# Kernel tuning notes

Hardware: AMD Instinct MI355X
Metric: run time of the kernel (lower is better)

## Reference

```python
import jax, jax.numpy as jnp
import numpy as np

B, S, D, H, L, V = 2, 512, 1024, 16, 12, 50257
HD = D // H
DFF = 4 * D


def _ln(x, g, b, eps=1e-5):
    m = jnp.mean(x, axis=-1, keepdims=True)
    v = jnp.var(x, axis=-1, keepdims=True)
    return (x - m) * jax.lax.rsqrt(v + eps) * g + b


def setup_inputs() -> dict:
    key = jax.random.key(0)
    ks = jax.random.split(key, 32)
    sc = 0.02
    n = lambda k, shape: (jax.random.normal(k, shape, dtype=jnp.float32) * sc)
    inp = {
        "input_ids": jax.random.randint(ks[0], (B, S), 0, V, dtype=jnp.int64),
        "attention_mask": jnp.ones((B, S), dtype=jnp.float32),
        "image_hidden_states": jax.random.normal(ks[1], (B, D), dtype=jnp.float32),
        # token embedding table (also used for position embeds and tied lm_head, as in source)
        "wte": n(ks[2], (V, D)),
        # feature_space_transformation_nn: Linear(1024,1024) -> ReLU -> Linear(1024,1024)
        "ft_W1": n(ks[3], (D, D)), "ft_b1": jnp.zeros((D,), jnp.float32),
        "ft_W2": n(ks[4], (D, D)), "ft_b2": jnp.zeros((D,), jnp.float32),
        # per-layer params, stacked on leading L dim
        "ln1_g": jnp.ones((L, D), jnp.float32), "ln1_b": jnp.zeros((L, D), jnp.float32),
        "Wattn": n(ks[5], (L, D, 3 * D)), "battn": jnp.zeros((L, 3 * D), jnp.float32),
        "Wuk": n(ks[6], (L, D, D)), "buk": jnp.zeros((L, D), jnp.float32),
        "Wuv": n(ks[7], (L, D, D)), "buv": jnp.zeros((L, D), jnp.float32),
        "Wproj": n(ks[8], (L, D, D)), "bproj": jnp.zeros((L, D), jnp.float32),
        "ln2_g": jnp.ones((L, D), jnp.float32), "ln2_b": jnp.zeros((L, D), jnp.float32),
        "Wfc": n(ks[9], (L, D, DFF)), "bfc": jnp.zeros((L, DFF), jnp.float32),
        "Wfc2": n(ks[10], (L, DFF, D)), "bfc2": jnp.zeros((L, D), jnp.float32),
        "lnf_g": jnp.ones((D,), jnp.float32), "lnf_b": jnp.zeros((D,), jnp.float32),
    }
    return inp


def _forward(input_ids, attention_mask, image_hidden_states, wte,
             ft_W1, ft_b1, ft_W2, ft_b2,
             ln1_g, ln1_b, Wattn, battn, Wuk, buk, Wuv, buv, Wproj, bproj,
             ln2_g, ln2_b, Wfc, bfc, Wfc2, bfc2, lnf_g, lnf_b):
    # image feature transformation: Linear -> ReLU -> Linear
    img = jax.nn.relu(image_hidden_states @ ft_W1 + ft_b1) @ ft_W2 + ft_b2  # [B,D]

    # NOTE: source uses wte (not wpe) for position embeddings — faithful reproduction
    h = wte[input_ids] + wte[jnp.arange(S)][None]  # [B,S,D]

    # extended attention mask with a prepended zero column for the image token
    mask_ext = (1.0 - attention_mask)[:, None, None, :] * -10000.0  # [B,1,1,S]
    mask_ext = jnp.concatenate([jnp.zeros((B, 1, 1, 1), mask_ext.dtype), mask_ext], axis=-1)  # [B,1,1,S+1]

    # causal mask over kv_len=S+1: query i sees keys j <= i+1 (image token always visible)
    causal = jnp.arange(S + 1)[None, :] <= (jnp.arange(S)[:, None] + 1)  # [S,S+1]

    def block(h, p):
        (l1g, l1b, Wa, ba, Wk, bk, Wv, bv, Wp, bp, l2g, l2b, Wf, bf, Wf2, bf2) = p
        x = _ln(h, l1g, l1b)
        qkv = x @ Wa + ba
        q, k, v = jnp.split(qkv, 3, axis=-1)  # each [B,S,D]
        ki = (img @ Wk + bk)[:, None, :]  # [B,1,D]
        vi = (img @ Wv + bv)[:, None, :]
        k = jnp.concatenate([ki, k], axis=1)  # [B,S+1,D]
        v = jnp.concatenate([vi, v], axis=1)
        sh = lambda t, n: t.reshape(B, n, H, HD).transpose(0, 2, 1, 3)
        qh, kh, vh = sh(q, S), sh(k, S + 1), sh(v, S + 1)
        s = jnp.einsum('bhqd,bhkd->bhqk', qh, kh) / jnp.sqrt(jnp.float32(HD))
        s = jnp.where(causal[None, None], s, jnp.float32(-10000.0))
        s = s + mask_ext
        a = jax.nn.softmax(s, axis=-1)
        o = jnp.einsum('bhqk,bhkd->bhqd', a, vh).transpose(0, 2, 1, 3).reshape(B, S, D)
        h = h + (o @ Wp + bp)
        x = _ln(h, l2g, l2b)
        h = h + (jax.nn.gelu(x @ Wf + bf, approximate=True) @ Wf2 + bf2)
        return h, None

    params = (ln1_g, ln1_b, Wattn, battn, Wuk, buk, Wuv, buv, Wproj, bproj,
              ln2_g, ln2_b, Wfc, bfc, Wfc2, bfc2)
    h, _ = jax.lax.scan(block, h, params)
    h = _ln(h, lnf_g, lnf_b)
    return h @ wte.T  # tied lm head -> [B,S,V]


def reference(input_ids, attention_mask, image_hidden_states, wte,
              ft_W1, ft_b1, ft_W2, ft_b2,
              ln1_g, ln1_b, Wattn, battn, Wuk, buk, Wuv, buv, Wproj, bproj,
              ln2_g, ln2_b, Wfc, bfc, Wfc2, bfc2, lnf_g, lnf_b):
    return _forward(input_ids, attention_mask, image_hidden_states, wte,
                    ft_W1, ft_b1, ft_W2, ft_b2,
                    ln1_g, ln1_b, Wattn, battn, Wuk, buk, Wuv, buv, Wproj, bproj,
                    ln2_g, ln2_b, Wfc, bfc, Wfc2, bfc2, lnf_g, lnf_b)
```

## Files before the change

### kernel.cpp

```cpp
#include <hip/hip_runtime.h>
#include <cstdint>


typedef __bf16 bf16x8 __attribute__((ext_vector_type(8)));
typedef __bf16 bf16x4 __attribute__((ext_vector_type(4)));
typedef float  f32x4  __attribute__((ext_vector_type(4)));

#define GLDS16(g, l) __builtin_amdgcn_global_load_lds( \
    (const __attribute__((address_space(1))) unsigned int*)(g), \
    (__attribute__((address_space(3))) unsigned int*)(l), 16, 0, 0)

#define SCHED_FENCE() __builtin_amdgcn_sched_barrier(0)

__device__ __forceinline__ float gelu_f(float x) {
    float u = 1.5957691216057308f * (x + 0.044715f * x * x * x);
    float e = __expf(u);
    float t = 1.0f - 2.0f / (e + 1.0f);
    return 0.5f * x * (1.0f + t);
}

__device__ __forceinline__ int fragoff(int row, int kh, int hi) {
    return row * 64 + ((kh * 32 + hi * 8) ^ ((row & 7) << 3));
}
__device__ __forceinline__ int fragoff32(int row, int hi) {
    return row * 32 + ((hi * 8) ^ ((row & 3) << 3));
}

__device__ __forceinline__ void tcvt_body(
    int id, const float* __restrict__ Wa, const float* __restrict__ Wp,
    const float* __restrict__ Wf, const float* __restrict__ Wf2,
    __bf16* __restrict__ oa, __bf16* __restrict__ op,
    __bf16* __restrict__ of, __bf16* __restrict__ of2, float* tile)
{
    const float* src; __bf16* dst; int K, N, kb, nb;
    if (id < 768)       { src = Wa;  dst = oa;  K = 1024; N = 3072; kb = id & 15; nb = id >> 4; }
    else if (id < 1024) { id -= 768;  src = Wp;  dst = op;  K = 1024; N = 1024; kb = id & 15; nb = id >> 4; }
    else if (id < 2048) { id -= 1024; src = Wf;  dst = of;  K = 1024; N = 4096; kb = id & 15; nb = id >> 4; }
    else                { id -= 2048; src = Wf2; dst = of2; K = 4096; N = 1024; kb = id & 63; nb = id >> 6; }
    const int k0 = kb * 64, n0 = nb * 64;
    const int t = threadIdx.x;
    #pragma unroll
    for (int i = 0; i < 4; i++) {
        int r = i * 16 + (t >> 4), c = (t & 15) * 4;
        float4 v = *reinterpret_cast<const float4*>(src + (long)(k0 + r) * N + n0 + c);
        tile[r * 65 + c] = v.x; tile[r * 65 + c + 1] = v.y;
        tile[r * 65 + c + 2] = v.z; tile[r * 65 + c + 3] = v.w;
    }
    __syncthreads();
    const int nrow = t >> 2, kc = (t & 3) * 16;
    bf16x8 o0, o1;
    #pragma unroll
    for (int i = 0; i < 8; i++) {
        o0[i] = (__bf16)tile[(kc + i) * 65 + nrow];
        o1[i] = (__bf16)tile[(kc + 8 + i) * 65 + nrow];
    }
    *reinterpret_cast<bf16x8*>(dst + (long)(n0 + nrow) * K + k0 + kc)     = o0;
    *reinterpret_cast<bf16x8*>(dst + (long)(n0 + nrow) * K + k0 + kc + 8) = o1;
}

__device__ __forceinline__ void wcvt_body(
    int id, const float* __restrict__ wte, __bf16* __restrict__ out, long nvalid)
{
    long base = (long)id * 8192 + threadIdx.x * 8;
    #pragma unroll
    for (int i = 0; i < 4; i++) {
        long e = base + (long)i * 2048;
        bf16x8 o;
        if (e < nvalid) {
            float4 a = *reinterpret_cast<const float4*>(wte + e);
            float4 b = *reinterpret_cast<const float4*>(wte + e + 4);
            o[0] = (__bf16)a.x; o[1] = (__bf16)a.y; o[2] = (__bf16)a.z; o[3] = (__bf16)a.w;
            o[4] = (__bf16)b.x; o[5] = (__bf16)b.y; o[6] = (__bf16)b.z; o[7] = (__bf16)b.w;
        } else {
            #pragma unroll
            for (int q = 0; q < 8; q++) o[q] = (__bf16)0.f;
        }
        *reinterpret_cast<bf16x8*>(out + e) = o;
    }
}

__global__ __launch_bounds__(256) void tcvt_std(
    const float* __restrict__ Wa, const float* __restrict__ Wp,
    const float* __restrict__ Wf, const float* __restrict__ Wf2,
    __bf16* __restrict__ oa, __bf16* __restrict__ op,
    __bf16* __restrict__ of, __bf16* __restrict__ of2)
{
    __shared__ float tile[64 * 65];
    tcvt_body(blockIdx.x, Wa, Wp, Wf, Wf2, oa, op, of, of2, tile);
}

__global__ __launch_bounds__(256) void wcvt_std(
    const float* __restrict__ wte, __bf16* __restrict__ out, long nvalid)
{
    wcvt_body(blockIdx.x, wte, out, nvalid);
}

__global__ __launch_bounds__(256) void gemv_part(
    const float* __restrict__ x, int xld,
    const float* __restrict__ W, long wzs,
    float* __restrict__ part, int K, int N)
{
    int jb = blockIdx.x, kz = blockIdx.y, z = blockIdx.z;
    int t = threadIdx.x;
    int j = (jb << 6) + (t & 63);
    int g = t >> 6;
    int klen = K / (gridDim.y * 4);
    int kbase = (kz * 4 + g) * klen;
    const float* Wp = W + (long)z * wzs + (long)kbase * N + j;
    const float* x0 = x + kbase;
    const float* x1 = x + xld + kbase;
    float a0 = 0.f, a1 = 0.f;
    for (int k = 0; k < klen; k++) {
        float wv = Wp[(long)k * N];
        a0 += x0[k] * wv;
        a1 += x1[k] * wv;
    }
    __shared__ float r0[4][64], r1[4][64];
    r0[g][t & 63] = a0; r1[g][t & 63] = a1;
    __syncthreads();
    if (t < 64) {
        a0 = r0[0][t] + r0[1][t] + r0[2][t] + r0[3][t];
        a1 = r1[0][t] + r1[1][t] + r1[2][t] + r1[3][t];
        long base = (long)(z * gridDim.y + kz) * 2 * N + (jb << 6) + t;
        part[base]     = a0;
        part[base + N] = a1;
    }
}

__global__ __launch_bounds__(256) void gemv_reduce(
    const float* __restrict__ part, const float* __restrict__ bias, long bzs,
    float* __restrict__ out, int N, int nz, int act)
{
    int idx = blockIdx.x * 256 + threadIdx.x;
    if (idx >= nz * 2 * N) return;
    int j  = idx % N;
    int bz = idx / N;
    int z  = bz >> 1;
    float s = bias[(long)z * bzs + j];
    const float* p = part + ((long)z * 8 * 2 + (bz & 1)) * N + j;
    #pragma unroll
    for (int kz = 0; kz < 8; kz++) s += p[(long)kz * 2 * N];
    if (act) s = fmaxf(s, 0.f);
    out[idx] = s;
}

__global__ __launch_bounds__(256) void gemv_kv_part(
    const float* __restrict__ img,
    const float* __restrict__ Wuk, const float* __restrict__ Wuv,
    float* __restrict__ part)
{
    int jb = blockIdx.x, kz = blockIdx.y, z = blockIdx.z;
    int t = threadIdx.x;
    int j = (jb << 6) + (t & 63);
    int g = t >> 6;
    int kbase = (kz * 4 + g) * 64;
    const float* W = (z < 12) ? (Wuk + (long)z * 1048576) : (Wuv + (long)(z - 12) * 1048576);
    const float* Wp = W + (long)kbase * 1024 + j;
    const float* x0 = img + kbase;
    const float* x1 = img + 1024 + kbase;
    float a0 = 0.f, a1 = 0.f;
    for (int k = 0; k < 64; k++) {
        float wv = Wp[(long)k * 1024];
        a0 += x0[k] * wv;
        a1 += x1[k] * wv;
    }
    __shared__ float r0[4][64], r1[4][64];
    r0[g][t & 63] = a0; r1[g][t & 63] = a1;
    __syncthreads();
    if (t < 64) {
        a0 = r0[0][t] + r0[1][t] + r0[2][t] + r0[3][t];
        a1 = r1[0][t] + r1[1][t] + r1[2][t] + r1[3][t];
        long base = (long)(z * 4 + kz) * 2 * 1024 + (jb << 6) + t;
        part[base]        = a0;
        part[base + 1024] = a1;
    }
}

__global__ __launch_bounds__(256) void gemv_kv_reduce(
    const float* __restrict__ part,
    const float* __restrict__ buk, const float* __restrict__ buv,
    float* __restrict__ imgk, float* __restrict__ imgv)
{
    int idx = blockIdx.x * 256 + threadIdx.x;
    int z = idx >> 11;
    int bsel = (idx >> 10) & 1;
    int j = idx & 1023;
    float s = (z < 12) ? buk[z * 1024 + j] : buv[(z - 12) * 1024 + j];
    const float* p = part + ((long)z * 4 * 2 + bsel) * 1024 + j;
    #pragma unroll
    for (int kz = 0; kz < 4; kz++) s += p[(long)kz * 2 * 1024];
    if (z < 12) imgk[z * 2048 + bsel * 1024 + j] = s;
    else        imgv[(z - 12) * 2048 + bsel * 1024 + j] = s;
}

__global__ __launch_bounds__(256) void embed_ln(
    const int* __restrict__ ids, const float* __restrict__ wte,
    float* __restrict__ h, __bf16* __restrict__ xb,
    const float* __restrict__ g, const float* __restrict__ b)
{
    int row = blockIdx.x;
    int s = row & 511;
    int t = threadIdx.x;
    long id = ids[row];
    float4 v1 = reinterpret_cast<const float4*>(wte + id * 1024)[t];
    float4 v2 = reinterpret_cast<const float4*>(wte + (long)s * 1024)[t];
    float4 v; v.x = v1.x + v2.x; v.y = v1.y + v2.y; v.z = v1.z + v2.z; v.w = v1.w + v2.w;
    reinterpret_cast<float4*>(h + (long)row * 1024)[t] = v;

    float s1 = v.x + v.y + v.z + v.w;
    float s2 = v.x * v.x + v.y * v.y + v.z * v.z + v.w * v.w;
    #pragma unroll
    for (int o = 32; o >= 1; o >>= 1) { s1 += __shfl_xor(s1, o); s2 += __shfl_xor(s2, o); }
    __shared__ float r1[4], r2[4];
    int w = t >> 6;
    if ((t & 63) == 0) { r1[w] = s1; r2[w] = s2; }
    __syncthreads();
    s1 = r1[0] + r1[1] + r1[2] + r1[3];
    s2 = r2[0] + r2[1] + r2[2] + r2[3];
    float mean = s1 * (1.0f / 1024.0f);
    float var  = s2 * (1.0f / 1024.0f) - mean * mean;
    float rstd = rsqrtf(var + 1e-5f);
    float4 gg = reinterpret_cast<const float4*>(g)[t];
    float4 bb = reinterpret_cast<const float4*>(b)[t];
    bf16x4 o;
    o[0] = (__bf16)((v.x - mean) * rstd * gg.x + bb.x);
    o[1] = (__bf16)((v.y - mean) * rstd * gg.y + bb.y);
    o[2] = (__bf16)((v.z - mean) * rstd * gg.z + bb.z);
    o[3] = (__bf16)((v.w - mean) * rstd * gg.w + bb.w);
    *reinterpret_cast<bf16x4*>(xb + (long)row * 1024 + t * 4) = o;
}

__global__ __launch_bounds__(256) void ln_k(
    const float* __restrict__ in, __bf16* __restrict__ out,
    const float* __restrict__ g, const float* __restrict__ b)
{
    int row = blockIdx.x, t = threadIdx.x;
    float4 v = reinterpret_cast<const float4*>(in + (long)row * 1024)[t];
    float s1 = v.x + v.y + v.z + v.w;
    float s2 = v.x * v.x + v.y * v.y + v.z * v.z + v.w * v.w;
    #pragma unroll
    for (int o = 32; o >= 1; o >>= 1) { s1 += __shfl_xor(s1, o); s2 += __shfl_xor(s2, o); }
    __shared__ float r1[4], r2[4];
    int w = t >> 6;
    if ((t & 63) == 0) { r1[w] = s1; r2[w] = s2; }
    __syncthreads();
    s1 = r1[0] + r1[1] + r1[2] + r1[3];
    s2 = r2[0] + r2[1] + r2[2] + r2[3];
    float mean = s1 * (1.0f / 1024.0f);
    float var  = s2 * (1.0f / 1024.0f) - mean * mean;
    float rstd = rsqrtf(var + 1e-5f);
    float4 gg = reinterpret_cast<const float4*>(g)[t];
    float4 bb = reinterpret_cast<const float4*>(b)[t];
    bf16x4 o;
    o[0] = (__bf16)((v.x - mean) * rstd * gg.x + bb.x);
    o[1] = (__bf16)((v.y - mean) * rstd * gg.y + bb.y);
    o[2] = (__bf16)((v.z - mean) * rstd * gg.z + bb.z);
    o[3] = (__bf16)((v.w - mean) * rstd * gg.w + bb.w);
    *reinterpret_cast<bf16x4*>(out + (long)row * 1024 + t * 4) = o;
}

template<int NP>
__global__ __launch_bounds__(256) void lnadd_k(
    float* __restrict__ h, const float* __restrict__ part,
    const float* __restrict__ bias,
    const float* __restrict__ g, const float* __restrict__ b,
    __bf16* __restrict__ out)
{
    int row = blockIdx.x, t = threadIdx.x;
    long off = (long)row * 1024 + t * 4;
    float4 v = *reinterpret_cast<const float4*>(h + off);
    #pragma unroll
    for (int sp = 0; sp < NP; sp++) {
        float4 pv = *reinterpret_cast<const float4*>(part + sp * 1048576L + off);
        v.x += pv.x; v.y += pv.y; v.z += pv.z; v.w += pv.w;
    }
    float4 bi = reinterpret_cast<const float4*>(bias)[t];
    v.x += bi.x; v.y += bi.y; v.z += bi.z; v.w += bi.w;
    *reinterpret_cast<float4*>(h + off) = v;

    float s1 = v.x + v.y + v.z + v.w;
    float s2 = v.x * v.x + v.y * v.y + v.z * v.z + v.w * v.w;
    #pragma unroll
    for (int o = 32; o >= 1; o >>= 1) { s1 += __shfl_xor(s1, o); s2 += __shfl_xor(s2, o); }
    __shared__ float r1[4], r2[4];
    int w = t >> 6;
    if ((t & 63) == 0) { r1[w] = s1; r2[w] = s2; }
    __syncthreads();
    s1 = r1[0] + r1[1] + r1[2] + r1[3];
    s2 = r2[0] + r2[1] + r2[2] + r2[3];
    float mean = s1 * (1.0f / 1024.0f);
    float var  = s2 * (1.0f / 1024.0f) - mean * mean;
    float rstd = rsqrtf(var + 1e-5f);
    float4 gg = reinterpret_cast<const float4*>(g)[t];
    float4 bb = reinterpret_cast<const float4*>(b)[t];
    bf16x4 o;
    o[0] = (__bf16)((v.x - mean) * rstd * gg.x + bb.x);
    o[1] = (__bf16)((v.y - mean) * rstd * gg.y + bb.y);
    o[2] = (__bf16)((v.z - mean) * rstd * gg.z + bb.z);
    o[3] = (__bf16)((v.w - mean) * rstd * gg.w + bb.w);
    *reinterpret_cast<bf16x4*>(out + off) = o;
}

__global__ __launch_bounds__(512, 4) void gemm_lm2(
    const __bf16* __restrict__ A, const __bf16* __restrict__ Bt,
    float* __restrict__ C, int N, int K, int GM, int GN)
{
    const int total = GM * GN;
    const int q = total >> 3, r = total & 7;
    const int x = blockIdx.x & 7, jj = blockIdx.x >> 3;
    const int w0 = (x < r) ? x * (q + 1) + jj : r * (q + 1) + (x - r) * q + jj;
    const int m0 = (w0 % GM) * 128;
    const int n0 = (w0 / GM) * 256;

    __shared__ __bf16 As[2][128 * 32];
    __shared__ __bf16 Bs[2][256 * 32];
    const int t = threadIdx.x;
    const int wid = t >> 6, lane = t & 63;
    const int lo = lane & 15, hi = lane >> 4;
    const int wr = wid >> 2, wc = wid & 3;

    f32x4 acc[4][4] = {};

    const int srow = t >> 2;
    const int skx  = (((t & 3) ^ (srow & 3)) << 3);
    const int sldst = t * 8;
    #define STLM(bf, kk) do { \
        GLDS16(A + (long)(m0 + srow) * K + (kk) + skx, &As[bf][sldst]); \
        GLDS16(Bt + (long)(n0 + srow)       * K + (kk) + skx, &Bs[bf][sldst]); \
        GLDS16(Bt + (long)(n0 + 128 + srow) * K + (kk) + skx, &Bs[bf][4096 + sldst]); \
    } while (0)

    const int T = K >> 5;
    STLM(0, 0);
    int cur = 0;
    for (int it = 0; it < T; it++) {
        if (it + 1 < T) {
            STLM(cur ^ 1, (it + 1) * 32);
            asm volatile("s_waitcnt vmcnt(3)" ::: "memory");
        } else {
            asm volatile("s_waitcnt vmcnt(0)" ::: "memory");
        }
        SCHED_FENCE();
        __builtin_amdgcn_s_barrier();
        SCHED_FENCE();

        bf16x8 afr[4], bfr[4];
        #pragma unroll
        for (int mi = 0; mi < 4; mi++)
            afr[mi] = *reinterpret_cast<const bf16x8*>(&As[cur][fragoff32(wr * 64 + mi * 16 + lo, hi)]);
        #pragma unroll
        for (int ni = 0; ni < 4; ni++)
            bfr[ni] = *reinterpret_cast<const bf16x8*>(&Bs[cur][fragoff32(wc * 64 + ni * 16 + lo, hi)]);
        __builtin_amdgcn_s_setprio(1);
        #pragma unroll
        for (int mi = 0; mi < 4; mi++)
            #pragma unroll
            for (int ni = 0; ni < 4; ni++)
                acc[mi][ni] = __builtin_amdgcn_mfma_f32_16x16x32_bf16(afr[mi], bfr[ni], acc[mi][ni], 0, 0, 0);
        __builtin_amdgcn_s_setprio(0);

        SCHED_FENCE();
        __builtin_amdgcn_s_barrier();
        SCHED_FENCE();
        cur ^= 1;
    }
    #undef STLM

    #pragma unroll
    for (int mi = 0; mi < 4; mi++)
        #pragma unroll
        for (int ni = 0; ni < 4; ni++) {
            int col = n0 + wc * 64 + ni * 16 + lo;
            if (col >= N) continue;
            #pragma unroll
            for (int rr = 0; rr < 4; rr++) {
                int row = m0 + wr * 64 + mi * 16 + hi * 4 + rr;
                C[(long)row * N + col] = acc[mi][ni][rr];
            }
        }
}

template<int BN, int OUTBF16, int ACT, int PARTIAL>
__global__ __launch_bounds__(256) void gemm64(
    const __bf16* __restrict__ A, const __bf16* __restrict__ Bt,
    const float* __restrict__ bias, void* __restrict__ C,
    int N, int K, int GM, int GN, int NS)
{
    constexpr int NB = BN / 32;
    const int total = GM * GN * NS;
    const int q = total >> 3, r = total & 7;
    const int x = blockIdx.x & 7, jj = blockIdx.x >> 3;
    const int w0 = (x < r) ? x * (q + 1) + jj : r * (q + 1) + (x - r) * q + jj;
    const int sp = w0 / (GM * GN);
    const int rem = w0 - sp * (GM * GN);
    const int m0 = (rem % GM) * 64;
    const int n0 = (rem / GM) * BN;

    __shared__ __bf16 As[2][64 * 64];
    __shared__ __bf16 Bs[2][BN * 64];
    const int t = threadIdx.x;
    const int wv = t >> 6, lane = t & 63;
    const int lo = lane & 15, hi = lane >> 4;
    const int wr = wv >> 1, wc = wv & 1;

    f32x4 acc[2][NB] = {};

    const int srow = t >> 3;
    const int skx  = (((t & 7) ^ (srow & 7)) << 3);
    const int sldst = t * 8;
    #define ST64(bf, kk) do { \
        _Pragma("unroll") \
        for (int i = 0; i < 2; i++) \
            GLDS16(A + (long)(m0 + i * 32 + srow) * K + (kk) + skx, &As[bf][i * 2048 + sldst]); \
        _Pragma("unroll") \
        for (int i = 0; i < NB; i++) \
            GLDS16(Bt + (long)(n0 + i * 32 + srow) * K + (kk) + skx, &Bs[bf][i * 2048 + sldst]); \
    } while (0)

    const int Ksp = K / NS;
    const int kbeg = sp * Ksp;
    const int T = Ksp >> 6;

    ST64(0, kbeg);
    int cur = 0;
    for (int it = 0; it < T; it++) {
        if (it + 1 < T) {
            ST64(cur ^ 1, kbeg + (it + 1) * 64);
            if constexpr (NB == 4) asm volatile("s_waitcnt vmcnt(6)" ::: "memory");
            else                   asm volatile("s_waitcnt vmcnt(4)" ::: "memory");
        } else {
            asm volatile("s_waitcnt vmcnt(0)" ::: "memory");
        }
        SCHED_FENCE();
        __builtin_amdgcn_s_barrier();
        SCHED_FENCE();

        #pragma unroll
        for (int kh = 0; kh < 2; kh++) {
            bf16x8 afr[2], bfr[NB];
            #pragma unroll
            for (int mi = 0; mi < 2; mi++)
                afr[mi] = *reinterpret_cast<const bf16x8*>(&As[cur][fragoff(wr * 32 + mi * 16 + lo, kh, hi)]);
            #pragma unroll
            for (int ni = 0; ni < NB; ni++)
                bfr[ni] = *reinterpret_cast<const bf16x8*>(&Bs[cur][fragoff(wc * (BN / 2) + ni * 16 + lo, kh, hi)]);
            __builtin_amdgcn_s_setprio(1);
            #pragma unroll
            for (int mi = 0; mi < 2; mi++)
                #pragma unroll
                for (int ni = 0; ni < NB; ni++)
                    acc[mi][ni] = __builtin_amdgcn_mfma_f32_16x16x32_bf16(afr[mi], bfr[ni], acc[mi][ni], 0, 0, 0);
            __builtin_amdgcn_s_setprio(0);
        }

        SCHED_FENCE();
        __builtin_amdgcn_s_barrier();
        SCHED_FENCE();
        cur ^= 1;
    }
    #undef ST64

    const long coff = PARTIAL ? (long)sp * GM * 64 * N : 0;
    #pragma unroll
    for (int mi = 0; mi < 2; mi++)
        #pragma unroll
        for (int ni = 0; ni < NB; ni++) {
            int col = n0 + wc * (BN / 2) + ni * 16 + lo;
            float bv = (!PARTIAL && bias) ? bias[col] : 0.f;
            #pragma unroll
            for (int rr = 0; rr < 4; rr++) {
                int row = m0 + wr * 32 + mi * 16 + hi * 4 + rr;
                float v = acc[mi][ni][rr] + bv;
                if (ACT) v = gelu_f(v);
                if (OUTBF16) ((__bf16*)C)[(long)row * N + col] = (__bf16)v;
                else         ((float*)C)[coff + (long)row * N + col] = v;
            }
        }
}

template<int OUTBF16, int ACT, int RES>
__global__ __launch_bounds__(256) void gemm_bb(
    const __bf16* __restrict__ A, const __bf16* __restrict__ Bt,
    const float* __restrict__ bias, const float* __restrict__ res,
    void* __restrict__ C, int N, int K)
{
    __shared__ __bf16 As[64 * 32];
    __shared__ __bf16 Bs[64 * 32];
    const int t = threadIdx.x;
    const int m0 = blockIdx.x * 64;
    const int n0 = blockIdx.y * 64;
    const int w = t >> 6, lane = t & 63;
    const int lo = lane & 15, hi = lane >> 4;
    const int wr = w >> 1, wc = w & 1;

    f32x4 acc[2][2] = {};

    for (int k0 = 0; k0 < K; k0 += 32) {
        __syncthreads();
        GLDS16(A  + (long)(m0 + (t >> 2)) * K + k0 + ((t & 3) << 3), &As[t * 8]);
        GLDS16(Bt + (long)(n0 + (t >> 2)) * K + k0 + ((t & 3) << 3), &Bs[t * 8]);
        __syncthreads();
        bf16x8 afr[2], bfr[2];
        #pragma unroll
        for (int mi = 0; mi < 2; mi++)
            afr[mi] = *reinterpret_cast<const bf16x8*>(&As[(wr * 32 + mi * 16 + lo) * 32 + hi * 8]);
        #pragma unroll
        for (int ni = 0; ni < 2; ni++)
            bfr[ni] = *reinterpret_cast<const bf16x8*>(&Bs[(wc * 32 + ni * 16 + lo) * 32 + hi * 8]);
        #pragma unroll
        for (int mi = 0; mi < 2; mi++)
            #pragma unroll
            for (int ni = 0; ni < 2; ni++)
                acc[mi][ni] = __builtin_amdgcn_mfma_f32_16x16x32_bf16(afr[mi], bfr[ni], acc[mi][ni], 0, 0, 0);
    }

    #pragma unroll
    for (int mi = 0; mi < 2; mi++)
        #pragma unroll
        for (int ni = 0; ni < 2; ni++) {
            int col = n0 + wc * 32 + ni * 16 + lo;
            float bv = bias ? bias[col] : 0.f;
            #pragma unroll
            for (int rr = 0; rr < 4; rr++) {
                int row = m0 + wr * 32 + mi * 16 + hi * 4 + rr;
                float v = acc[mi][ni][rr] + bv;
                if (ACT) v = gelu_f(v);
                if (RES) v += res[(long)row * N + col];
                if (OUTBF16) ((__bf16*)C)[(long)row * N + col] = (__bf16)v;
                else         ((float*)C)[(long)row * N + col] = v;
            }
        }
}

__global__ __launch_bounds__(256) void gemm_lm(
    const __bf16* __restrict__ A, const float* __restrict__ Wt,
    float* __restrict__ C, int N, int K)
{
    __shared__ __bf16 As[128 * 32];
    __shared__ __bf16 Bs[128 * 32];
    const int t = threadIdx.x;
    const int m0 = blockIdx.x * 128;
    const int n0 = blockIdx.y * 128;
    const int w = t >> 6, lane = t & 63;
    const int lo = lane & 15, hi = lane >> 4;
    const int wr = w >> 1, wc = w & 1;

    f32x4 acc[4][4] = {};

    for (int k0 = 0; k0 < K; k0 += 32) {
        __syncthreads();
        #pragma unroll
        for (int i = 0; i < 2; i++) {
            int c = i * 256 + t;
            GLDS16(A + (long)(m0 + (c >> 2)) * K + k0 + ((c & 3) << 3), &As[c * 8]);
        }
        #pragma unroll
        for (int i = 0; i < 2; i++) {
            int c = i * 256 + t;
            int nr = n0 + (c >> 2);
            bf16x8 bv;
            if (nr < N) {
                const float* wp = Wt + (long)nr * K + k0 + ((c & 3) << 3);
                float4 b0 = *reinterpret_cast<const float4*>(wp);
                float4 b1 = *reinterpret_cast<const float4*>(wp + 4);
                bv[0] = (__bf16)b0.x; bv[1] = (__bf16)b0.y; bv[2] = (__bf16)b0.z; bv[3] = (__bf16)b0.w;
                bv[4] = (__bf16)b1.x; bv[5] = (__bf16)b1.y; bv[6] = (__bf16)b1.z; bv[7] = (__bf16)b1.w;
            } else {
                #pragma unroll
                for (int qq = 0; qq < 8; qq++) bv[qq] = (__bf16)0.f;
            }
            *reinterpret_cast<bf16x8*>(&Bs[c * 8]) = bv;
        }
        __syncthreads();
        bf16x8 afr[4], bfr[4];
        #pragma unroll
        for (int mi = 0; mi < 4; mi++)
            afr[mi] = *reinterpret_cast<const bf16x8*>(&As[(wr * 64 + mi * 16 + lo) * 32 + hi * 8]);
        #pragma unroll
        for (int ni = 0; ni < 4; ni++)
            bfr[ni] = *reinterpret_cast<const bf16x8*>(&Bs[(wc * 64 + ni * 16 + lo) * 32 + hi * 8]);
        #pragma unroll
        for (int mi = 0; mi < 4; mi++)
            #pragma unroll
            for (int ni = 0; ni < 4; ni++)
                acc[mi][ni] = __builtin_amdgcn_mfma_f32_16x16x32_bf16(afr[mi], bfr[ni], acc[mi][ni], 0, 0, 0);
    }

    #pragma unroll
    for (int mi = 0; mi < 4; mi++)
        #pragma unroll
        for (int ni = 0; ni < 4; ni++) {
            int col = n0 + wc * 64 + ni * 16 + lo;
            if (col < N) {
                #pragma unroll
                for (int rr = 0; rr < 4; rr++) {
                    int row = m0 + wr * 64 + mi * 16 + hi * 4 + rr;
                    C[(long)row * N + col] = acc[mi][ni][rr];
                }
            }
        }
}

__global__ __launch_bounds__(256) void attn_aux(
    const __bf16* __restrict__ qkv,
    const float* __restrict__ imgk, const float* __restrict__ imgv,
    const float* __restrict__ amask, __bf16* __restrict__ out,
    int aux_mode,
    const float* __restrict__ Wa, const float* __restrict__ Wp,
    const float* __restrict__ Wf, const float* __restrict__ Wf2,
    __bf16* __restrict__ oa, __bf16* __restrict__ op,
    __bf16* __restrict__ of, __bf16* __restrict__ of2,
    const float* __restrict__ wte, __bf16* __restrict__ wteb, long nvalid)
{
    __shared__ __align__(16) char smem[28416];
    const int bid = blockIdx.x;
    if (bid >= 256) {
        if (aux_mode == 1)
            tcvt_body(bid - 256, Wa, Wp, Wf, Wf2, oa, op, of, of2, (float*)smem);
        else
            wcvt_body(bid - 256, wte, wteb, nvalid);
        return;
    }

    __bf16 (*Ks)[72] = (__bf16(*)[72])(smem);
    __bf16 (*Vt)[72] = (__bf16(*)[72])(smem + 9216);
    __bf16 (*Ps)[16][72] = (__bf16(*)[16][72])(smem + 18432);
    float* kimg_s = (float*)(smem + 27648);
    float* amv_s  = (float*)(smem + 27904);

    const int qb = bid & 7;
    const int h  = (bid >> 3) & 15;
    const int b  = bid >> 7;
    const int t = threadIdx.x, w = t >> 6, lane = t & 63;
    const int lo = lane & 15, hi = lane >> 4;

    const int kr8 = t >> 2, kd8 = (t & 3) * 16;
    const int vr8 = t & 63, vd8 = (t >> 6) * 16;

    const __bf16* qrow = qkv + (long)(b * 512 + qb * 64 + w * 16 + lo) * 3072 + h * 64;
    bf16x8 qf0 = *reinterpret_cast<const bf16x8*>(qrow + hi * 8);
    bf16x8 qf1 = *reinterpret_cast<const bf16x8*>(qrow + 32 + hi * 8);

    if (t < 64) kimg_s[t] = imgk[b * 1024 + h * 64 + t];
    __syncthreads();

    float simg = 0.f;
    #pragma unroll
    for (int i = 0; i < 8; i++)
        simg += (float)qf0[i] * kimg_s[hi * 8 + i] + (float)qf1[i] * kimg_s[32 + hi * 8 + i];
    simg += __shfl_xor(simg, 16);
    simg += __shfl_xor(simg, 32);
    simg *= 0.125f;

    float pimg[4], l_part[4];
    f32x4 o_acc[4];
    #pragma unroll
    for (int rr = 0; rr < 4; rr++) {
        pimg[rr] = __expf(__shfl(simg, hi * 4 + rr));
        l_part[rr] = 0.f;
    }
    #pragma unroll
    for (int df = 0; df < 4; df++) {
        float vi = imgv[b * 1024 + h * 64 + df * 16 + lo];
        #pragma unroll
        for (int rr = 0; rr < 4; rr++) o_acc[df][rr] = pimg[rr] * vi;
    }

    bf16x8 ck0, ck1, cv0, cv1;
    {
        const __bf16* ks = qkv + (long)(b * 512 + kr8) * 3072 + 1024 + h * 64 + kd8;
        ck0 = *reinterpret_cast<const bf16x8*>(ks);
        ck1 = *reinterpret_cast<const bf16x8*>(ks + 8);
        const __bf16* vs = qkv + (long)(b * 512 + vr8) * 3072 + 2048 + h * 64 + vd8;
        cv0 = *reinterpret_cast<const bf16x8*>(vs);
        cv1 = *reinterpret_cast<const bf16x8*>(vs + 8);
    }

    for (int kb = 0; kb <= qb; kb++) {
        bf16x8 nk0, nk1, nv0, nv1;
        const bool more = (kb < qb);
        if (more) {
            const __bf16* ks = qkv + (long)(b * 512 + (kb + 1) * 64 + kr8) * 3072 + 1024 + h * 64 + kd8;
            nk0 = *reinterpret_cast<const bf16x8*>(ks);
            nk1 = *reinterpret_cast<const bf16x8*>(ks + 8);
            const __bf16* vs = qkv + (long)(b * 512 + (kb + 1) * 64 + vr8) * 3072 + 2048 + h * 64 + vd8;
            nv0 = *reinterpret_cast<const bf16x8*>(vs);
            nv1 = *reinterpret_cast<const bf16x8*>(vs + 8);
        }
        __syncthreads();
        *reinterpret_cast<bf16x8*>(&Ks[kr8][kd8])     = ck0;
        *reinterpret_cast<bf16x8*>(&Ks[kr8][kd8 + 8]) = ck1;
        #pragma unroll
        for (int i = 0; i < 8; i++) { Vt[vd8 + i][vr8] = cv0[i]; Vt[vd8 + 8 + i][vr8] = cv1[i]; }
        if (t < 64) amv_s[t] = (1.0f - amask[b * 512 + kb * 64 + t]) * -10000.0f;
        __syncthreads();

        f32x4 sf[4];
        #pragma unroll
        for (int js = 0; js < 4; js++) {
            bf16x8 kf0 = *reinterpret_cast<const bf16x8*>(&Ks[js * 16 + lo][hi * 8]);
            bf16x8 kf1 = *reinterpret_cast<const bf16x8*>(&Ks[js * 16 + lo][32 + hi * 8]);
            f32x4 a = {};
            a = __builtin_amdgcn_mfma_f32_16x16x32_bf16(qf0, kf0, a, 0, 0, 0);
            a = __builtin_amdgcn_mfma_f32_16x16x32_bf16(qf1, kf1, a, 0, 0, 0);
            sf[js] = a;
        }
        #pragma unroll
        for (int js = 0; js < 4; js++) {
            float amv = amv_s[js * 16 + lo];
            #pragma unroll
            for (int rr = 0; rr < 4; rr++) {
                float sv = sf[js][rr] * 0.125f + amv;
                if (kb == qb) {
                    int qrw = w * 16 + hi * 4 + rr;
                    if (js * 16 + lo > qrw) sv = -10000.0f + amv;
                }
                float p = __expf(sv);
                l_part[rr] += p;
                Ps[w][hi * 4 + rr][js * 16 + lo] = (__bf16)p;
            }
        }
        #pragma unroll
        for (int jb = 0; jb < 2; jb++) {
            bf16x8 pf = *reinterpret_cast<const bf16x8*>(&Ps[w][lo][jb * 32 + hi * 8]);
            #pragma unroll
            for (int df = 0; df < 4; df++) {
                bf16x8 vf = *reinterpret_cast<const bf16x8*>(&Vt[df * 16 + lo][jb * 32 + hi * 8]);
                o_acc[df] = __builtin_amdgcn_mfma_f32_16x16x32_bf16(pf, vf, o_acc[df], 0, 0, 0);
            }
        }
        if (more) { ck0 = nk0; ck1 = nk1; cv0 = nv0; cv1 = nv1; }
    }

    float linv[4];
    #pragma unroll
    for (int rr = 0; rr < 4; rr++) {
        float ls = l_part[rr];
        #pragma unroll
        for (int off = 1; off < 16; off <<= 1) ls += __shfl_xor(ls, off);
        linv[rr] = 1.0f / (pimg[rr] + ls);
    }
    #pragma unroll
    for (int df = 0; df < 4; df++)
        #pragma unroll
        for (int rr = 0; rr < 4; rr++) {
            long row = b * 512 + qb * 64 + w * 16 + hi * 4 + rr;
            out[row * 1024 + h * 64 + df * 16 + lo] = (__bf16)(o_acc[df][rr] * linv[rr]);
        }
}

extern "C" void kernel_launch(void* const* d_in, const int* in_sizes, int n_in,
                              void* d_out, int out_size, void* d_ws, size_t ws_size,
                              hipStream_t stream) {
    (void)in_sizes; (void)n_in; (void)out_size;
    const int*   ids   = (const int*)d_in[0];
    const float* amask = (const float*)d_in[1];
    const float* ihs   = (const float*)d_in[2];
    const float* wte   = (const float*)d_in[3];
    const float* ftW1  = (const float*)d_in[4];
    const float* ftb1  = (const float*)d_in[5];
    const float* ftW2  = (const float*)d_in[6];
    const float* ftb2  = (const float*)d_in[7];
    const float* ln1g  = (const float*)d_in[8];
    const float* ln1b  = (const float*)d_in[9];
    const float* Wattn = (const float*)d_in[10];
    const float* battn = (const float*)d_in[11];
    const float* Wuk   = (const float*)d_in[12];
    const float* buk   = (const float*)d_in[13];
    const float* Wuv   = (const float*)d_in[14];
    const float* buv   = (const float*)d_in[15];
    const float* Wproj = (const float*)d_in[16];
    const float* bproj = (const float*)d_in[17];
    const float* ln2g  = (const float*)d_in[18];
    const float* ln2b  = (const float*)d_in[19];
    const float* Wfc   = (const float*)d_in[20];
    const float* bfc   = (const float*)d_in[21];
    const float* Wfc2  = (const float*)d_in[22];
    const float* bfc2  = (const float*)d_in[23];
    const float* lnfg  = (const float*)d_in[24];
    const float* lnfb  = (const float*)d_in[25];
    float* out = (float*)d_out;

    const long VP2 = 50432;
    const long NVALID = 50257L * 1024;
    char* base = (char*)d_ws;
    float* ftmp  = (float*)(base);
    float* img   = (float*)(base + (1 << 13));
    float* imgk  = (float*)(base + (1 << 14));
    float* imgv  = (float*)(base + 114688);
    float* part  = (float*)(base + 212992);
    float* h     = (float*)(base + 1048576);
    char* p = base + 5 * 1048576;
    __bf16* xb    = (__bf16*)p; p += 2 * 1048576;
    __bf16* qkvb  = (__bf16*)p; p += 6 * 1048576;
    __bf16* attob = (__bf16*)p; p += 2 * 1048576;
    __bf16* ffb   = (__bf16*)p; p += 8 * 1048576;
    __bf16* wtA0  = (__bf16*)p; p += 6 * 1048576;
    __bf16* wtP0  = (__bf16*)p; p += 2 * 1048576;
    __bf16* wtF0  = (__bf16*)p; p += 8 * 1048576;
    __bf16* wtF20 = (__bf16*)p; p += 8 * 1048576;
    __bf16* wteb  = (__bf16*)p; p += VP2 * 1024 * 2;
    size_t need1 = (size_t)(p - base);
    float* part_g = (float*)(base + need1);
    size_t need2 = need1 + 4 * 1048576 * sizeof(float);
    char* p2 = base + need2;
    __bf16* wtA1  = (__bf16*)p2; p2 += 6 * 1048576;
    __bf16* wtP1  = (__bf16*)p2; p2 += 2 * 1048576;
    __bf16* wtF1  = (__bf16*)p2; p2 += 8 * 1048576;
    __bf16* wtF21 = (__bf16*)p2; p2 += 8 * 1048576;
    size_t need3 = (size_t)(p2 - base);
    const bool big1 = (ws_size >= need1);
    const bool big2 = (ws_size >= need2);
    const bool big3 = (ws_size >= need3);

    __bf16* wtA_s[2]  = {wtA0, wtA1};
    __bf16* wtP_s[2]  = {wtP0, wtP1};
    __bf16* wtF_s[2]  = {wtF0, wtF1};
    __bf16* wtF2_s[2] = {wtF20, wtF21};

    dim3 b256(256);

    gemv_part<<<dim3(16, 8, 1), b256, 0, stream>>>(ihs, 1024, ftW1, 0, part, 1024, 1024);
    gemv_reduce<<<dim3(8), b256, 0, stream>>>(part, ftb1, 0, ftmp, 1024, 1, 1);
    gemv_part<<<dim3(16, 8, 1), b256, 0, stream>>>(ftmp, 1024, ftW2, 0, part, 1024, 1024);
    gemv_reduce<<<dim3(8), b256, 0, stream>>>(part, ftb2, 0, img, 1024, 1, 0);
    gemv_kv_part<<<dim3(16, 4, 24), b256, 0, stream>>>(img, Wuk, Wuv, part);
    gemv_kv_reduce<<<dim3(192), b256, 0, stream>>>(part, buk, buv, imgk, imgv);

    embed_ln<<<dim3(1024), b256, 0, stream>>>(ids, wte, h, xb, ln1g, ln1b);
    tcvt_std<<<dim3(3072), b256, 0, stream>>>(
        Wattn, Wproj, Wfc, Wfc2, wtA0, wtP0, wtF0, wtF20);

    for (int l = 0; l < 12; l++) {
        const int cs = big3 ? (l & 1) : 0;
        __bf16* cA  = wtA_s[cs];
        __bf16* cP  = wtP_s[cs];
        __bf16* cF  = wtF_s[cs];
        __bf16* cF2 = wtF2_s[cs];

        if (!big3 && l > 0) {
            tcvt_std<<<dim3(3072), b256, 0, stream>>>(
                Wattn + (long)l * 1024 * 3072, Wproj + (long)l * 1024 * 1024,
                Wfc + (long)l * 1024 * 4096, Wfc2 + (long)l * 4096 * 1024,
                wtA0, wtP0, wtF0, wtF20);
        }

        gemm64<128, 1, 0, 0><<<dim3(384), b256, 0, stream>>>(
            xb, cA, battn + l * 3072, qkvb, 3072, 1024, 16, 24, 1);

        if (big3 && l < 11) {
            const int ns = (l + 1) & 1;
            attn_aux<<<dim3(256 + 3072), b256, 0, stream>>>(
                qkvb, imgk + l * 2048, imgv + l * 2048, amask, attob, 1,
                Wattn + (long)(l + 1) * 1024 * 3072, Wproj + (long)(l + 1) * 1024 * 1024,
                Wfc + (long)(l + 1) * 1024 * 4096, Wfc2 + (long)(l + 1) * 4096 * 1024,
                wtA_s[ns], wtP_s[ns], wtF_s[ns], wtF2_s[ns],
                nullptr, nullptr, 0);
        } else if (big3 && l == 11) {
            attn_aux<<<dim3(256 + 6304), b256, 0, stream>>>(
                qkvb, imgk + l * 2048, imgv + l * 2048, amask, attob, 2,
                nullptr, nullptr, nullptr, nullptr,
                nullptr, nullptr, nullptr, nullptr,
                wte, wteb, NVALID);
        } else {
            attn_aux<<<dim3(256), b256, 0, stream>>>(
                qkvb, imgk + l * 2048, imgv + l * 2048, amask, attob, 0,
                nullptr, nullptr, nullptr, nullptr,
                nullptr, nullptr, nullptr, nullptr,
                nullptr, nullptr, 0);
        }

        const float* ng = (l < 11) ? (ln1g + (l + 1) * 1024) : lnfg;
        const float* nb = (l < 11) ? (ln1b + (l + 1) * 1024) : lnfb;
        if (big2) {
            gemm64<64, 0, 0, 1><<<dim3(512), b256, 0, stream>>>(
                attob, cP, nullptr, part_g, 1024, 1024, 16, 16, 2);
            lnadd_k<2><<<dim3(1024), b256, 0, stream>>>(
                h, part_g, bproj + l * 1024, ln2g + l * 1024, ln2b + l * 1024, xb);
            gemm64<128, 1, 1, 0><<<dim3(512), b256, 0, stream>>>(
                xb, cF, bfc + l * 4096, ffb, 4096, 1024, 16, 32, 1);
            gemm64<128, 0, 0, 1><<<dim3(512), b256, 0, stream>>>(
                ffb, cF2, nullptr, part_g, 1024, 4096, 16, 8, 4);
            lnadd_k<4><<<dim3(1024), b256, 0, stream>>>(
                h, part_g, bfc2 + l * 1024, ng, nb, xb);
        } else {
            gemm_bb<0, 0, 1><<<dim3(16, 16), b256, 0, stream>>>(
                attob, cP, bproj + l * 1024, h, h, 1024, 1024);
            ln_k<<<dim3(1024), b256, 0, stream>>>(h, xb, ln2g + l * 1024, ln2b + l * 1024);
            gemm64<128, 1, 1, 0><<<dim3(512), b256, 0, stream>>>(
                xb, cF, bfc + l * 4096, ffb, 4096, 1024, 16, 32, 1);
            gemm_bb<0, 0, 1><<<dim3(16, 16), b256, 0, stream>>>(
                ffb, cF2, bfc2 + l * 1024, h, h, 1024, 4096);
            ln_k<<<dim3(1024), b256, 0, stream>>>(h, xb, ng, nb);
        }
    }

    if (big1) {
        if (!big3)
            wcvt_std<<<dim3((unsigned)(VP2 * 1024 / 8192)), b256, 0, stream>>>(wte, wteb, NVALID);
        gemm_lm2<<<dim3(8 * (int)(VP2 / 256)), dim3(512), 0, stream>>>(
            xb, wteb, out, 50257, 1024, 8, (int)(VP2 / 256));
    } else {
        gemm_lm<<<dim3(8, 393), b256, 0, stream>>>(xb, wte, out, 50257, 1024);
    }
}
```

Measured before the change: 1.477 ms.

## Triple-buffer LDS prefetch in GEMM kernels and change lm-head LDS swizzle

Both the lm-head GEMM and the generic 64-row GEMM move from double to triple buffering in shared memory, so loads for two k-steps ahead are in flight and the vmcnt wait thresholds are adjusted to match. The lm-head kernel's 32-wide LDS swizzle now XORs on (row>>1)&3 instead of row&3, aimed at reducing bank conflicts in fragment reads. The extra buffer raises LDS use per block by half, which may lower occupancy, especially for the 512-thread lm-head kernel with launch bounds of 4 blocks.

```diff
diff --git a/kernel.cpp b/kernel.cpp
--- a/kernel.cpp
+++ b/kernel.cpp
@@ -23,7 +23,7 @@
     return row * 64 + ((kh * 32 + hi * 8) ^ ((row & 7) << 3));
 }
 __device__ __forceinline__ int fragoff32(int row, int hi) {
-    return row * 32 + ((hi * 8) ^ ((row & 3) << 3));
+    return row * 32 + ((hi ^ ((row >> 1) & 3)) << 3);
 }
 
 __device__ __forceinline__ void tcvt_body(
@@ -312,8 +312,8 @@
     const int m0 = (w0 % GM) * 128;
     const int n0 = (w0 / GM) * 256;
 
-    __shared__ __bf16 As[2][128 * 32];
-    __shared__ __bf16 Bs[2][256 * 32];
+    __shared__ __bf16 As[3][128 * 32];
+    __shared__ __bf16 Bs[3][256 * 32];
     const int t = threadIdx.x;
     const int wid = t >> 6, lane = t & 63;
     const int lo = lane & 15, hi = lane >> 4;
@@ -322,7 +322,7 @@
     f32x4 acc[4][4] = {};
 
     const int srow = t >> 2;
-    const int skx  = (((t & 3) ^ (srow & 3)) << 3);
+    const int skx  = (((t & 3) ^ ((srow >> 1) & 3)) << 3);
     const int sldst = t * 8;
     #define STLM(bf, kk) do { \
         GLDS16(A + (long)(m0 + srow) * K + (kk) + skx, &As[bf][sldst]); \
@@ -332,10 +332,14 @@
 
     const int T = K >> 5;
     STLM(0, 0);
-    int cur = 0;
+    if (T > 1) STLM(1, 32);
+    int bcur = 0;
     for (int it = 0; it < T; it++) {
-        if (it + 1 < T) {
-            STLM(cur ^ 1, (it + 1) * 32);
+        if (it + 2 < T) {
+            int bst = bcur >= 1 ? bcur - 1 : bcur + 2;
+            STLM(bst, (it + 2) * 32);
+            asm volatile("s_waitcnt vmcnt(6)" ::: "memory");
+        } else if (it + 1 < T) {
             asm volatile("s_waitcnt vmcnt(3)" ::: "memory");
         } else {
             asm volatile("s_waitcnt vmcnt(0)" ::: "memory");
@@ -347,10 +351,10 @@
         bf16x8 afr[4], bfr[4];
         #pragma unroll
         for (int mi = 0; mi < 4; mi++)
-            afr[mi] = *reinterpret_cast<const bf16x8*>(&As[cur][fragoff32(wr * 64 + mi * 16 + lo, hi)]);
+            afr[mi] = *reinterpret_cast<const bf16x8*>(&As[bcur][fragoff32(wr * 64 + mi * 16 + lo, hi)]);
         #pragma unroll
         for (int ni = 0; ni < 4; ni++)
-            bfr[ni] = *reinterpret_cast<const bf16x8*>(&Bs[cur][fragoff32(wc * 64 + ni * 16 + lo, hi)]);
+            bfr[ni] = *reinterpret_cast<const bf16x8*>(&Bs[bcur][fragoff32(wc * 64 + ni * 16 + lo, hi)]);
         __builtin_amdgcn_s_setprio(1);
         #pragma unroll
         for (int mi = 0; mi < 4; mi++)
@@ -362,7 +366,7 @@
         SCHED_FENCE();
         __builtin_amdgcn_s_barrier();
         SCHED_FENCE();
-        cur ^= 1;
+        bcur = bcur < 2 ? bcur + 1 : 0;
     }
     #undef STLM
 
@@ -387,6 +391,7 @@
     int N, int K, int GM, int GN, int NS)
 {
     constexpr int NB = BN / 32;
+    constexpr int LP = 2 + NB;
     const int total = GM * GN * NS;
     const int q = total >> 3, r = total & 7;
     const int x = blockIdx.x & 7, jj = blockIdx.x >> 3;
@@ -396,8 +401,8 @@
     const int m0 = (rem % GM) * 64;
     const int n0 = (rem / GM) * BN;
 
-    __shared__ __bf16 As[2][64 * 64];
-    __shared__ __bf16 Bs[2][BN * 64];
+    __shared__ __bf16 As[3][64 * 64];
+    __shared__ __bf16 Bs[3][BN * 64];
     const int t = threadIdx.x;
     const int wv = t >> 6, lane = t & 63;
     const int lo = lane & 15, hi = lane >> 4;
@@ -422,12 +427,15 @@
     const int T = Ksp >> 6;
 
     ST64(0, kbeg);
-    int cur = 0;
+    if (T > 1) ST64(1, kbeg + 64);
+    int bcur = 0;
     for (int it = 0; it < T; it++) {
-        if (it + 1 < T) {
-            ST64(cur ^ 1, kbeg + (it + 1) * 64);
-            if constexpr (NB == 4) asm volatile("s_waitcnt vmcnt(6)" ::: "memory");
-            else                   asm volatile("s_waitcnt vmcnt(4)" ::: "memory");
+        if (it + 2 < T) {
+            int bst = bcur >= 1 ? bcur - 1 : bcur + 2;
+            ST64(bst, kbeg + (it + 2) * 64);
+            asm volatile("s_waitcnt vmcnt(%0)" :: "i"(2 * LP) : "memory");
+        } else if (it + 1 < T) {
+            asm volatile("s_waitcnt vmcnt(%0)" :: "i"(LP) : "memory");
         } else {
             asm volatile("s_waitcnt vmcnt(0)" ::: "memory");
         }
@@ -440,10 +448,10 @@
             bf16x8 afr[2], bfr[NB];
             #pragma unroll
             for (int mi = 0; mi < 2; mi++)
-                afr[mi] = *reinterpret_cast<const bf16x8*>(&As[cur][fragoff(wr * 32 + mi * 16 + lo, kh, hi)]);
+                afr[mi] = *reinterpret_cast<const bf16x8*>(&As[bcur][fragoff(wr * 32 + mi * 16 + lo, kh, hi)]);
             #pragma unroll
             for (int ni = 0; ni < NB; ni++)
-                bfr[ni] = *reinterpret_cast<const bf16x8*>(&Bs[cur][fragoff(wc * (BN / 2) + ni * 16 + lo, kh, hi)]);
+                bfr[ni] = *reinterpret_cast<const bf16x8*>(&Bs[bcur][fragoff(wc * (BN / 2) + ni * 16 + lo, kh, hi)]);
             __builtin_amdgcn_s_setprio(1);
             #pragma unroll
             for (int mi = 0; mi < 2; mi++)
@@ -456,7 +464,7 @@
         SCHED_FENCE();
         __builtin_amdgcn_s_barrier();
         SCHED_FENCE();
-        cur ^= 1;
+        bcur = bcur < 2 ? bcur + 1 : 0;
     }
     #undef ST64
 
```

New measurement: 1.461 ms. No clear change (-1.1%).
